# Optimization experiments

Hardware: AMD Instinct MI355X
Metric: run time of the kernel (lower is better)

Reference implementation:

```python
import jax, jax.numpy as jnp
import numpy as np

EPS = 1e-5

def layer_norm(x, w, b):
    mu = x.mean(-1, keepdims=True)
    var = x.var(-1, keepdims=True)
    return (x - mu) / jnp.sqrt(var + EPS) * w + b

def s5_forward(u, Lambda_re, Lambda_im, B_re, B_im, C_re, C_im, D, log_step):
    # u: [B, L, H]; diagonal S5 SSM with P complex states, ZOH discretization.
    Lam = (Lambda_re + 1j * Lambda_im).astype(jnp.complex64)          # [P]
    dt = jnp.exp(log_step).astype(jnp.complex64)                       # [P]
    Lam_bar = jnp.exp(Lam * dt)                                        # [P]
    Bc = (B_re + 1j * B_im).astype(jnp.complex64)                      # [P, H]
    B_bar = ((Lam_bar - 1.0) / Lam)[:, None] * Bc                      # [P, H]
    Bu = jnp.einsum('blh,ph->blp', u.astype(jnp.complex64), B_bar)     # [B, L, P]
    A = jnp.broadcast_to(Lam_bar, Bu.shape)                            # [B, L, P]

    def binop(e1, e2):
        a1, b1 = e1
        a2, b2 = e2
        return (a2 * a1, a2 * b1 + b2)

    _, xs = jax.lax.associative_scan(binop, (A, Bu), axis=1)           # [B, L, P]
    Cc = (C_re + 1j * C_im).astype(jnp.complex64)                      # [H, P]
    y = 2.0 * jnp.einsum('blp,hp->blh', xs, Cc).real + D * u           # [B, L, H]
    return y

def setup_inputs() -> dict:
    key = jax.random.key(0)
    ks = jax.random.split(key, 12)
    B, L, H, P = 4, 4096, 512, 512
    x = jax.random.normal(ks[0], (B, L, H), jnp.float32)
    # SSM params (HiPPO-like flavor: negative real part, spread imaginary part)
    Lambda_re = -(0.5 * jax.random.uniform(ks[1], (P,), jnp.float32) + 0.1)
    Lambda_im = jnp.pi * jnp.arange(P, dtype=jnp.float32)
    B_re = jax.random.normal(ks[2], (P, H), jnp.float32) / np.sqrt(2.0 * H)
    B_im = jax.random.normal(ks[3], (P, H), jnp.float32) / np.sqrt(2.0 * H)
    C_re = jax.random.normal(ks[4], (H, P), jnp.float32) / np.sqrt(P)
    C_im = jax.random.normal(ks[5], (H, P), jnp.float32) / np.sqrt(P)
    D = jax.random.normal(ks[6], (H,), jnp.float32)
    log_step = jax.random.uniform(ks[7], (P,), jnp.float32,
                                  minval=np.log(1e-3), maxval=np.log(1e-1))
    ln1_w = jnp.ones((H,), jnp.float32); ln1_b = jnp.zeros((H,), jnp.float32)
    ln2_w = jnp.ones((H,), jnp.float32); ln2_b = jnp.zeros((H,), jnp.float32)
    W_enc = jax.random.normal(ks[8], (2 * H, H), jnp.float32) / np.sqrt(H)
    W_dec = jax.random.normal(ks[9], (H, H), jnp.float32) / np.sqrt(H)
    return {"x": x, "ln1_w": ln1_w, "ln1_b": ln1_b,
            "Lambda_re": Lambda_re, "Lambda_im": Lambda_im,
            "B_re": B_re, "B_im": B_im, "C_re": C_re, "C_im": C_im,
            "D": D, "log_step": log_step,
            "ln2_w": ln2_w, "ln2_b": ln2_b, "W_enc": W_enc, "W_dec": W_dec}

def reference(x, ln1_w, ln1_b, Lambda_re, Lambda_im, B_re, B_im, C_re, C_im,
              D, log_step, ln2_w, ln2_b, W_enc, W_dec):
    fx = layer_norm(x, ln1_w, ln1_b)
    res = fx
    u = s5_forward(fx, Lambda_re, Lambda_im, B_re, B_im, C_re, C_im, D, log_step)
    h = jax.nn.gelu(u, approximate=False) + res  # eval mode: dropout = identity
    fx2 = layer_norm(h, ln2_w, ln2_b)
    e = fx2 @ W_enc.T                              # [B, L, 2H]
    a, g = jnp.split(e, 2, axis=-1)
    ff = a * jax.nn.gelu(g, approximate=False)     # GEGLU
    out = ff @ W_dec.T + fx2
    return out
```

## Files before the change

### kernel.cpp

```cpp
#include <hip/hip_runtime.h>
#include <math.h>

#define Bz 4
#define Lz 4096
#define Hz 512
#define Pz 512
#define Nz (Bz*Lz)
#define CL 32
#define NC (Lz/CL)
#define CS (Bz*NC*Pz)
#define EPSf 1e-5f

typedef unsigned short u16;
typedef unsigned int   u32;
typedef __attribute__((ext_vector_type(8))) short bf16x8;
typedef __attribute__((ext_vector_type(8))) short short8v;
typedef __attribute__((ext_vector_type(4))) float f32x4;

__device__ __forceinline__ float gelu_exact(float x){
    return 0.5f * x * (1.0f + erff(x * 0.70710678118654752f));
}
__device__ __forceinline__ u16 f2b(float f){
    union { float f; u32 u; } v; v.f = f;
    u32 u = v.u;
    u32 r = (u + 0x7FFFu + ((u >> 16) & 1u)) >> 16;
    return (u16)r;
}
__device__ __forceinline__ float b2f(u16 h){
    union { u32 u; float f; } v; v.u = ((u32)h) << 16; return v.f;
}

__device__ __forceinline__ void gload_lds16(const u16* g, u16* l){
    __builtin_amdgcn_global_load_lds(
        (const __attribute__((address_space(1))) void*)g,
        (__attribute__((address_space(3))) void*)l, 16, 0, 0);
}

__device__ __forceinline__ void load8(const float* p, float* v){
    f32x4 a = *(const f32x4*)p, c = *(const f32x4*)(p+4);
    #pragma unroll
    for (int j=0;j<4;++j){ v[j]=a[j]; v[4+j]=c[j]; }
}
__device__ __forceinline__ void load8(const u16* p, float* v){
    short8v s = *(const short8v*)p;
    #pragma unroll
    for (int j=0;j<8;++j) v[j] = b2f((u16)s[j]);
}

__global__ void setup_kernel(const float* __restrict__ Lre, const float* __restrict__ Lim,
                             const float* __restrict__ log_step,
                             float* __restrict__ prm){
    int p = blockIdx.x*blockDim.x + threadIdx.x;
    if (p >= Pz) return;
    float lr = Lre[p], li = Lim[p];
    float dt = expf(log_step[p]);
    float ar = lr*dt, ai = li*dt;
    float e = expf(ar);
    float Abr = e*cosf(ai), Abi = e*sinf(ai);
    prm[p]        = Abr;
    prm[Pz + p]   = Abi;
    float nr = Abr - 1.0f, ni = Abi;
    float d2 = lr*lr + li*li;
    prm[2*Pz + p] = (nr*lr + ni*li)/d2;
    prm[3*Pz + p] = (ni*lr - nr*li)/d2;
    float arC = ar*(float)CL, aiC = ai*(float)CL;
    float eC = expf(arC);
    prm[4*Pz + p] = eC*cosf(aiC);
    prm[5*Pz + p] = eC*sinf(aiC);
}

__global__ __launch_bounds__(256) void cvt_all(const float* __restrict__ B_re,
                                               const float* __restrict__ B_im,
                                               const float* __restrict__ C_re,
                                               const float* __restrict__ C_im,
                                               const float* __restrict__ W_enc,
                                               const float* __restrict__ W_dec,
                                               u16* __restrict__ Bcat,
                                               u16* __restrict__ Ccat,
                                               u16* __restrict__ Wenc,
                                               u16* __restrict__ Wdec){
    const int Q = 512*512;
    int i = blockIdx.x*256 + threadIdx.x;
    if (i < Q){ int p=i>>9, h=i&511; Bcat[(size_t)(2*p)*512 + h]   = f2b(B_re[i]); return; }
    i -= Q;
    if (i < Q){ int p=i>>9, h=i&511; Bcat[(size_t)(2*p+1)*512 + h] = f2b(B_im[i]); return; }
    i -= Q;
    if (i < Q){
        int h = i >> 9, p = i & 511;
        Ccat[(size_t)h*1024 + 2*p]     = f2b(C_re[i]);
        Ccat[(size_t)h*1024 + 2*p + 1] = f2b(-C_im[i]);
        return;
    }
    i -= Q;
    if (i < 2*Q){ Wenc[i] = f2b(W_enc[i]); return; }
    i -= 2*Q;
    Wdec[i] = f2b(W_dec[i]);
}

template<typename T>
__global__ __launch_bounds__(256) void ln_kernel(const T* __restrict__ in,
                                                 const float* __restrict__ w,
                                                 const float* __restrict__ b,
                                                 u16* __restrict__ ob){
    int row = blockIdx.x*4 + (threadIdx.x >> 6);
    int l = threadIdx.x & 63;
    float v[8];
    load8(in + (size_t)row*Hz + l*8, v);
    float s = 0.f, q = 0.f;
    #pragma unroll
    for (int j=0;j<8;++j){ s += v[j]; q += v[j]*v[j]; }
    #pragma unroll
    for (int o=32;o;o>>=1){ s += __shfl_xor(s,o); q += __shfl_xor(q,o); }
    float mu = s * (1.0f/512.0f);
    float rs = rsqrtf(q * (1.0f/512.0f) - mu*mu + EPSf);
    short8v o8;
    #pragma unroll
    for (int j=0;j<8;++j){
        int m = l*8 + j;
        o8[j] = (short)f2b((v[j]-mu)*rs*w[m] + b[m]);
    }
    *(short8v*)&ob[(size_t)row*Hz + l*8] = o8;
}

#define EY    1
#define ERES  2
#define EGLU  3
#define ESCAN 4

#define ATW (256*64)
#define BTW (128*64)
#define TBW (ATW+BTW)

__device__ __forceinline__ void stageA256v(const u16* __restrict__ src, int ld,
                                           int row0, int kt, u16* lds){
    int lane = threadIdx.x & 63, w = threadIdx.x >> 6;
    #pragma unroll
    for (int q=0;q<4;++q){
        int c = w + q*8;
        int r = c*8 + (lane >> 3);
        int colE = 8*((lane & 7) ^ ((lane >> 3) & 7));
        gload_lds16(src + (size_t)(row0 + r)*ld + kt + colE, lds + c*512);
    }
}
__device__ __forceinline__ void stageB128v(const u16* __restrict__ src, int ld,
                                           int row0, int kt, u16* lds){
    int lane = threadIdx.x & 63, w = threadIdx.x >> 6;
    #pragma unroll
    for (int q=0;q<2;++q){
        int c = w + q*8;
        int r = c*8 + (lane >> 3);
        int colE = 8*((lane & 7) ^ ((lane >> 3) & 7));
        gload_lds16(src + (size_t)(row0 + r)*ld + kt + colE, lds + c*512);
    }
}
__device__ __forceinline__ void stageBglu(const u16* __restrict__ Wenc, int fb,
                                          int kt, u16* lds){
    int lane = threadIdx.x & 63, w = threadIdx.x >> 6;
    #pragma unroll
    for (int q=0;q<2;++q){
        int c = w + q*8;
        int v = c*8 + (lane >> 3);
        int vf = v >> 4, r = v & 15;
        int grow = ((vf & 1) ? 512 : 0) + fb + (vf >> 1)*16 + r;
        int colE = 8*((lane & 7) ^ ((lane >> 3) & 7));
        gload_lds16(Wenc + (size_t)grow*512 + kt + colE, lds + c*512);
    }
}

template<int K, int EPI>
__global__ __launch_bounds__(512)
void gemmv(const u16* __restrict__ A, const u16* __restrict__ Bw, int M,
           u16* __restrict__ outB,
           const u16* __restrict__ fxB,
           const float* __restrict__ Dv,
           const u16* __restrict__ resB,
           float* __restrict__ outF,
           const float* __restrict__ prm,
           float* __restrict__ ERe,
           float* __restrict__ EIm)
{
    constexpr int NT = K/64;
    __shared__ u16 LDS[3*TBW];

    int nx = gridDim.x, ny = gridDim.y;
    int nwg = nx*ny;
    int lid = blockIdx.x + blockIdx.y*nx;
    int cpx = nwg >> 3;
    int gdx = (lid & 7)*cpx + (lid >> 3);
    int n0 = (gdx / ny) * 256;
    int mb = gdx % ny;
    int m0 = mb * 128;
    int fb = mb * 64;

    int l = threadIdx.x & 63;
    int w = threadIdx.x >> 6;
    int wm = w >> 1, wn = w & 1;
    int rb = wm*64, cb = wn*64;
    int lrow  = l & 15;
    int lcol0 = ((l >> 4)*8) ^ ((l & 7) << 3);
    int lcol1 = lcol0 ^ 32;

    f32x4 acc[4][4];
    #pragma unroll
    for (int i=0;i<4;++i)
        #pragma unroll
        for (int j=0;j<4;++j) acc[i][j] = (f32x4)(0.f);

    stageA256v(A, K, n0, 0, &LDS[0]);
    if (EPI==EGLU) stageBglu(Bw, fb, 0, &LDS[ATW]); else stageB128v(Bw, K, m0, 0, &LDS[ATW]);
    stageA256v(A, K, n0, 64, &LDS[TBW]);
    if (EPI==EGLU) stageBglu(Bw, fb, 64, &LDS[TBW+ATW]); else stageB128v(Bw, K, m0, 64, &LDS[TBW+ATW]);

    for (int T=0; T<NT; ++T){
        if (T == NT-1){ asm volatile("s_waitcnt vmcnt(0)" ::: "memory"); }
        else          { asm volatile("s_waitcnt vmcnt(6)" ::: "memory"); }
        __builtin_amdgcn_s_barrier();
        if (T+2 < NT){
            u16* buf = &LDS[((T+2)%3)*TBW];
            int ktn = (T+2)*64;
            stageA256v(A, K, n0, ktn, buf);
            if (EPI==EGLU) stageBglu(Bw, fb, ktn, buf+ATW); else stageB128v(Bw, K, m0, ktn, buf+ATW);
        }
        const u16* Ab = &LDS[(T%3)*TBW];
        const u16* Bb = Ab + ATW;
        bf16x8 a0[4], a1[4], b0[4], b1[4];
        #pragma unroll
        for (int f=0; f<4; ++f){
            a0[f] = *(const bf16x8*)&Ab[(rb + f*16 + lrow)*64 + lcol0];
            a1[f] = *(const bf16x8*)&Ab[(rb + f*16 + lrow)*64 + lcol1];
        }
        #pragma unroll
        for (int g=0; g<4; ++g){
            b0[g] = *(const bf16x8*)&Bb[(cb + g*16 + lrow)*64 + lcol0];
            b1[g] = *(const bf16x8*)&Bb[(cb + g*16 + lrow)*64 + lcol1];
        }
        __builtin_amdgcn_s_setprio(1);
        #pragma unroll
        for (int f=0; f<4; ++f)
            #pragma unroll
            for (int g=0; g<4; ++g){
                acc[f][g] = __builtin_amdgcn_mfma_f32_16x16x32_bf16(a0[f], b0[g], acc[f][g], 0,0,0);
                acc[f][g] = __builtin_amdgcn_mfma_f32_16x16x32_bf16(a1[f], b1[g], acc[f][g], 0,0,0);
            }
        __builtin_amdgcn_s_setprio(0);
    }

    int er = (l >> 4) * 4;
    int ec = l & 15;

    if (EPI == ESCAN){
        u16* gt = (u16*)LDS;
        __syncthreads();
        #pragma unroll
        for (int fm=0; fm<4; ++fm)
            #pragma unroll
            for (int g=0; g<4; ++g)
                #pragma unroll
                for (int q=0; q<4; ++q){
                    int rr = rb + fm*16 + er + q;
                    int cc = cb + g*16 + ec;
                    u16 hv = f2b(acc[fm][g][q]);
                    outB[(size_t)(n0 + rr)*M + (m0 + cc)] = hv;
                    gt[rr*128 + cc] = hv;
                }
        __syncthreads();
        int tid = threadIdx.x;
        int p = tid & 63, h = tid >> 6;
        int P = (m0 >> 1) + p;
        int b = n0 >> 12;
        int c = ((n0 & 4095) >> 5) + h;
        float Ar = prm[P], Ai = prm[Pz+P];
        float fre = prm[2*Pz+P], fim = prm[3*Pz+P];
        float xr = 0.f, xi = 0.f;
        int base = h*32*128 + 2*p;
        #pragma unroll 8
        for (int r = 0; r < 32; ++r){
            u32 v = *(const u32*)&gt[base + r*128];
            float gr = b2f((u16)(v & 0xffff));
            float gi = b2f((u16)(v >> 16));
            float br = fre*gr - fim*gi;
            float bi = fre*gi + fim*gr;
            float nr2 = Ar*xr - Ai*xi + br;
            float ni2 = Ar*xi + Ai*xr + bi;
            xr = nr2; xi = ni2;
        }
        size_t ci = ((size_t)(b*NC + c))*Pz + P;
        ERe[ci] = xr; EIm[ci] = xi;
    } else if (EPI == EGLU){
        #pragma unroll
        for (int fm=0; fm<4; ++fm)
            #pragma unroll
            for (int pr=0; pr<2; ++pr)
                #pragma unroll
                for (int q=0; q<4; ++q){
                    int n = n0 + rb + fm*16 + er + q;
                    int col = fb + (wn*2 + pr)*16 + ec;
                    float ffv = acc[fm][2*pr][q] * gelu_exact(acc[fm][2*pr+1][q]);
                    outB[(size_t)n*Hz + col] = f2b(ffv);
                }
    } else {
        #pragma unroll
        for (int fm=0; fm<4; ++fm)
            #pragma unroll
            for (int g=0; g<4; ++g)
                #pragma unroll
                for (int q=0; q<4; ++q){
                    int n = n0 + rb + fm*16 + er + q;
                    int m = m0 + cb + g*16 + ec;
                    float v = acc[fm][g][q];
                    if (EPI == EY){
                        size_t idx = (size_t)n*Hz + m;
                        float fxv = b2f(fxB[idx]);
                        float y = 2.0f*v + Dv[m]*fxv;
                        outB[idx] = f2b(gelu_exact(y) + fxv);
                    } else {
                        size_t idx = (size_t)n*Hz + m;
                        outF[idx] = v + b2f(resB[idx]);
                    }
                }
    }
}

__global__ __launch_bounds__(256) void scan_combine(const float* __restrict__ ERe,
                                                    const float* __restrict__ EIm,
                                                    const float* __restrict__ prm,
                                                    float* __restrict__ SinRe,
                                                    float* __restrict__ SinIm){
    int gt = blockIdx.x*256 + threadIdx.x;
    int b = gt / Pz, p = gt % Pz;
    float Ar = prm[4*Pz+p], Ai = prm[5*Pz+p];
    float Sr = 0.f, Si = 0.f;
    for (int c = 0; c < NC; ++c) {
        size_t idx = ((size_t)(b*NC + c))*Pz + p;
        SinRe[idx] = Sr; SinIm[idx] = Si;
        float er = ERe[idx], ei = EIm[idx];
        float nr = Ar*Sr - Ai*Si + er;
        float ni = Ar*Si + Ai*Sr + ei;
        Sr = nr; Si = ni;
    }
}

__global__ __launch_bounds__(64) void scan_phase2(u16* __restrict__ g,
                                                  const float* __restrict__ prm,
                                                  const float* __restrict__ SinRe,
                                                  const float* __restrict__ SinIm){
    int t = blockIdx.x;
    int ph = t & 1; t >>= 1;
    int c  = t % NC;
    int b  = t / NC;
    int p0 = ph*256 + threadIdx.x*4;
    int cbi = 2*p0;
    size_t base = ((size_t)(b*Lz + c*CL))*1024;
    size_t ci = ((size_t)(b*NC + c))*Pz + p0;
    float Ar[4], Ai[4], fr[4], fi[4], xr[4], xi[4];
    f32x4 sr4 = *(const f32x4*)&SinRe[ci];
    f32x4 si4 = *(const f32x4*)&SinIm[ci];
    #pragma unroll
    for (int j=0;j<4;++j){
        Ar[j]=prm[p0+j]; Ai[j]=prm[Pz+p0+j];
        fr[j]=prm[2*Pz+p0+j]; fi[j]=prm[3*Pz+p0+j];
        xr[j]=sr4[j]; xi[j]=si4[j];
    }
    for (int ll=0; ll<CL; ++ll){
        short8v v8 = *(const short8v*)&g[base + cbi];
        short8v o8;
        #pragma unroll
        for (int j=0;j<4;++j){
            float gr = b2f((u16)v8[2*j]), gi = b2f((u16)v8[2*j+1]);
            float br = fr[j]*gr - fi[j]*gi;
            float bi = fr[j]*gi + fi[j]*gr;
            float nr = Ar[j]*xr[j] - Ai[j]*xi[j] + br;
            float ni = Ar[j]*xi[j] + Ai[j]*xr[j] + bi;
            xr[j]=nr; xi[j]=ni;
            o8[2*j]   = (short)f2b(nr);
            o8[2*j+1] = (short)f2b(ni);
        }
        *(short8v*)&g[base + cbi] = o8;
        base += 1024;
    }
}

extern "C" void kernel_launch(void* const* d_in, const int* in_sizes, int n_in,
                              void* d_out, int out_size, void* d_ws, size_t ws_size,
                              hipStream_t stream) {
    const float* x        = (const float*)d_in[0];
    const float* ln1_w    = (const float*)d_in[1];
    const float* ln1_b    = (const float*)d_in[2];
    const float* Lre      = (const float*)d_in[3];
    const float* Lim      = (const float*)d_in[4];
    const float* B_re     = (const float*)d_in[5];
    const float* B_im     = (const float*)d_in[6];
    const float* C_re     = (const float*)d_in[7];
    const float* C_im     = (const float*)d_in[8];
    const float* Dv       = (const float*)d_in[9];
    const float* log_step = (const float*)d_in[10];
    const float* ln2_w    = (const float*)d_in[11];
    const float* ln2_b    = (const float*)d_in[12];
    const float* W_enc    = (const float*)d_in[13];
    const float* W_dec    = (const float*)d_in[14];
    float* out = (float*)d_out;

    const size_t NH = (size_t)Nz*Hz;
    char* W = (char*)d_ws;
    u16*   fxb  = (u16*)  (W);
    u16*   g    = (u16*)  (W + NH*2);
    u16*   hb   = (u16*)  (W + NH*6);
    u16*   fx2b = (u16*)  (W + NH*8);
    float* ERe  = (float*)(W + NH*10);
    float* EIm  = ERe + CS;
    float* SinRe= EIm + CS;
    float* SinIm= SinRe + CS;
    float* prm  = SinIm + CS;
    u16*   Bcat = (u16*)(prm + 6*Pz);
    u16*   Ccat = Bcat + 1024*512;
    u16*   Wenc = Ccat + 512*1024;
    u16*   Wdec = Wenc + 1024*512;

    setup_kernel<<<dim3(2), dim3(256), 0, stream>>>(Lre, Lim, log_step, prm);

    cvt_all<<<dim3(6*1024), dim3(256), 0, stream>>>(B_re, B_im, C_re, C_im, W_enc, W_dec,
                                                    Bcat, Ccat, Wenc, Wdec);

    ln_kernel<float><<<dim3(Nz/4), dim3(256), 0, stream>>>(x, ln1_w, ln1_b, fxb);

    gemmv<512,ESCAN><<<dim3(Nz/256, 1024/128), dim3(512), 0, stream>>>(
        fxb, Bcat, 1024, g, nullptr, nullptr, nullptr, nullptr, prm, ERe, EIm);

    scan_combine<<<dim3((Bz*Pz)/256), dim3(256), 0, stream>>>(ERe, EIm, prm, SinRe, SinIm);
    scan_phase2<<<dim3(Bz*NC*2), dim3(64), 0, stream>>>(g, prm, SinRe, SinIm);

    gemmv<1024,EY><<<dim3(Nz/256, 512/128), dim3(512), 0, stream>>>(
        g, Ccat, 512, hb, fxb, Dv, nullptr, nullptr, nullptr, nullptr, nullptr);

    ln_kernel<u16><<<dim3(Nz/4), dim3(256), 0, stream>>>(hb, ln2_w, ln2_b, fx2b);

    gemmv<512,EGLU><<<dim3(Nz/256, 1024/128), dim3(512), 0, stream>>>(
        fx2b, Wenc, 1024, fxb, nullptr, nullptr, nullptr, nullptr, nullptr, nullptr, nullptr);

    gemmv<512,ERES><<<dim3(Nz/256, 512/128), dim3(512), 0, stream>>>(
        fxb, Wdec, 512, nullptr, nullptr, nullptr, fx2b, out, nullptr, nullptr, nullptr);
}
```

Before: 169.2 us.

## Process two row tiles per GEGLU GEMM block, merge setup into conversion kernel

The GEGLU encoder GEMM now has each workgroup handle two consecutive 256-row tiles. The K loop runs across both tiles in one pipelined stream, and the first tile's GEGLU epilogue is written mid-loop before the accumulators are reset. This halves the grid and is meant to amortize pipeline fill and drain and the prologue cost, but the epilogue now stalls inside the pipeline. The setup kernel is folded into cvt_all as extra blocks to save a launch, and scan_combine uses 64-thread blocks to spread its 2048 serial threads over more CUs.

```diff
diff --git a/kernel.cpp b/kernel.cpp
--- a/kernel.cpp
+++ b/kernel.cpp
@@ -47,40 +47,43 @@
     for (int j=0;j<8;++j) v[j] = b2f((u16)s[j]);
 }
 
-__global__ void setup_kernel(const float* __restrict__ Lre, const float* __restrict__ Lim,
-                             const float* __restrict__ log_step,
-                             float* __restrict__ prm){
-    int p = blockIdx.x*blockDim.x + threadIdx.x;
-    if (p >= Pz) return;
-    float lr = Lre[p], li = Lim[p];
-    float dt = expf(log_step[p]);
-    float ar = lr*dt, ai = li*dt;
-    float e = expf(ar);
-    float Abr = e*cosf(ai), Abi = e*sinf(ai);
-    prm[p]        = Abr;
-    prm[Pz + p]   = Abi;
-    float nr = Abr - 1.0f, ni = Abi;
-    float d2 = lr*lr + li*li;
-    prm[2*Pz + p] = (nr*lr + ni*li)/d2;
-    prm[3*Pz + p] = (ni*lr - nr*li)/d2;
-    float arC = ar*(float)CL, aiC = ai*(float)CL;
-    float eC = expf(arC);
-    prm[4*Pz + p] = eC*cosf(aiC);
-    prm[5*Pz + p] = eC*sinf(aiC);
-}
-
 __global__ __launch_bounds__(256) void cvt_all(const float* __restrict__ B_re,
                                                const float* __restrict__ B_im,
                                                const float* __restrict__ C_re,
                                                const float* __restrict__ C_im,
                                                const float* __restrict__ W_enc,
                                                const float* __restrict__ W_dec,
+                                               const float* __restrict__ Lre,
+                                               const float* __restrict__ Lim,
+                                               const float* __restrict__ log_step,
                                                u16* __restrict__ Bcat,
                                                u16* __restrict__ Ccat,
                                                u16* __restrict__ Wenc,
-                                               u16* __restrict__ Wdec){
+                                               u16* __restrict__ Wdec,
+                                               float* __restrict__ prm){
     const int Q = 512*512;
-    int i = blockIdx.x*256 + threadIdx.x;
+    int blk = blockIdx.x;
+    if (blk >= 6*1024){
+        int p = (blk - 6*1024)*256 + threadIdx.x;
+        if (p >= Pz) return;
+        float lr = Lre[p], li = Lim[p];
+        float dt = expf(log_step[p]);
+        float ar = lr*dt, ai = li*dt;
+        float e = expf(ar);
+        float Abr = e*cosf(ai), Abi = e*sinf(ai);
+        prm[p]        = Abr;
+        prm[Pz + p]   = Abi;
+        float nr = Abr - 1.0f, ni = Abi;
+        float d2 = lr*lr + li*li;
+        prm[2*Pz + p] = (nr*lr + ni*li)/d2;
+        prm[3*Pz + p] = (ni*lr - nr*li)/d2;
+        float arC = ar*(float)CL, aiC = ai*(float)CL;
+        float eC = expf(arC);
+        prm[4*Pz + p] = eC*cosf(aiC);
+        prm[5*Pz + p] = eC*sinf(aiC);
+        return;
+    }
+    int i = blk*256 + threadIdx.x;
     if (i < Q){ int p=i>>9, h=i&511; Bcat[(size_t)(2*p)*512 + h]   = f2b(B_re[i]); return; }
     i -= Q;
     if (i < Q){ int p=i>>9, h=i&511; Bcat[(size_t)(2*p+1)*512 + h] = f2b(B_im[i]); return; }
@@ -180,6 +183,8 @@
            float* __restrict__ EIm)
 {
     constexpr int NT = K/64;
+    constexpr int NP = (EPI==EGLU) ? 2 : 1;
+    constexpr int TT = NT*NP;
     __shared__ u16 LDS[3*TBW];
 
     int nx = gridDim.x, ny = gridDim.y;
@@ -187,7 +192,7 @@
     int lid = blockIdx.x + blockIdx.y*nx;
     int cpx = nwg >> 3;
     int gdx = (lid & 7)*cpx + (lid >> 3);
-    int n0 = (gdx / ny) * 256;
+    int n0 = (gdx / ny) * 256 * NP;
     int mb = gdx % ny;
     int m0 = mb * 128;
     int fb = mb * 64;
@@ -199,6 +204,8 @@
     int lrow  = l & 15;
     int lcol0 = ((l >> 4)*8) ^ ((l & 7) << 3);
     int lcol1 = lcol0 ^ 32;
+    int er = (l >> 4) * 4;
+    int ec = l & 15;
 
     f32x4 acc[4][4];
     #pragma unroll
@@ -211,14 +218,16 @@
     stageA256v(A, K, n0, 64, &LDS[TBW]);
     if (EPI==EGLU) stageBglu(Bw, fb, 64, &LDS[TBW+ATW]); else stageB128v(Bw, K, m0, 64, &LDS[TBW+ATW]);
 
-    for (int T=0; T<NT; ++T){
-        if (T == NT-1){ asm volatile("s_waitcnt vmcnt(0)" ::: "memory"); }
+    for (int T=0; T<TT; ++T){
+        if (T == TT-1){ asm volatile("s_waitcnt vmcnt(0)" ::: "memory"); }
         else          { asm volatile("s_waitcnt vmcnt(6)" ::: "memory"); }
         __builtin_amdgcn_s_barrier();
-        if (T+2 < NT){
+        if (T+2 < TT){
             u16* buf = &LDS[((T+2)%3)*TBW];
-            int ktn = (T+2)*64;
-            stageA256v(A, K, n0, ktn, buf);
+            int t2 = T+2;
+            int ktn = (t2 % NT)*64;
+            int rowA = n0 + (t2/NT)*256;
+            stageA256v(A, K, rowA, ktn, buf);
             if (EPI==EGLU) stageBglu(Bw, fb, ktn, buf+ATW); else stageB128v(Bw, K, m0, ktn, buf+ATW);
         }
         const u16* Ab = &LDS[(T%3)*TBW];
@@ -243,10 +252,24 @@
                 acc[f][g] = __builtin_amdgcn_mfma_f32_16x16x32_bf16(a1[f], b1[g], acc[f][g], 0,0,0);
             }
         __builtin_amdgcn_s_setprio(0);
-    }
-
-    int er = (l >> 4) * 4;
-    int ec = l & 15;
+        if (EPI==EGLU && NP==2 && T == NT-1){
+            #pragma unroll
+            for (int fm=0; fm<4; ++fm)
+                #pragma unroll
+                for (int pr=0; pr<2; ++pr)
+                    #pragma unroll
+                    for (int q=0; q<4; ++q){
+                        int n = n0 + rb + fm*16 + er + q;
+                        int col = fb + (wn*2 + pr)*16 + ec;
+                        float ffv = acc[fm][2*pr][q] * gelu_exact(acc[fm][2*pr+1][q]);
+                        outB[(size_t)n*Hz + col] = f2b(ffv);
+                    }
+            #pragma unroll
+            for (int i=0;i<4;++i)
+                #pragma unroll
+                for (int j=0;j<4;++j) acc[i][j] = (f32x4)(0.f);
+        }
+    }
 
     if (EPI == ESCAN){
         u16* gt = (u16*)LDS;
@@ -287,13 +310,14 @@
         size_t ci = ((size_t)(b*NC + c))*Pz + P;
         ERe[ci] = xr; EIm[ci] = xi;
     } else if (EPI == EGLU){
+        int nb = n0 + (NP-1)*256;
         #pragma unroll
         for (int fm=0; fm<4; ++fm)
             #pragma unroll
             for (int pr=0; pr<2; ++pr)
                 #pragma unroll
                 for (int q=0; q<4; ++q){
-                    int n = n0 + rb + fm*16 + er + q;
+                    int n = nb + rb + fm*16 + er + q;
                     int col = fb + (wn*2 + pr)*16 + ec;
                     float ffv = acc[fm][2*pr][q] * gelu_exact(acc[fm][2*pr+1][q]);
                     outB[(size_t)n*Hz + col] = f2b(ffv);
@@ -321,12 +345,12 @@
     }
 }
 
-__global__ __launch_bounds__(256) void scan_combine(const float* __restrict__ ERe,
-                                                    const float* __restrict__ EIm,
-                                                    const float* __restrict__ prm,
-                                                    float* __restrict__ SinRe,
-                                                    float* __restrict__ SinIm){
-    int gt = blockIdx.x*256 + threadIdx.x;
+__global__ __launch_bounds__(64) void scan_combine(const float* __restrict__ ERe,
+                                                   const float* __restrict__ EIm,
+                                                   const float* __restrict__ prm,
+                                                   float* __restrict__ SinRe,
+                                                   float* __restrict__ SinIm){
+    int gt = blockIdx.x*64 + threadIdx.x;
     int b = gt / Pz, p = gt % Pz;
     float Ar = prm[4*Pz+p], Ai = prm[5*Pz+p];
     float Sr = 0.f, Si = 0.f;
@@ -416,17 +440,16 @@
     u16*   Wenc = Ccat + 512*1024;
     u16*   Wdec = Wenc + 1024*512;
 
-    setup_kernel<<<dim3(2), dim3(256), 0, stream>>>(Lre, Lim, log_step, prm);
-
-    cvt_all<<<dim3(6*1024), dim3(256), 0, stream>>>(B_re, B_im, C_re, C_im, W_enc, W_dec,
-                                                    Bcat, Ccat, Wenc, Wdec);
+    cvt_all<<<dim3(6*1024 + 2), dim3(256), 0, stream>>>(
+        B_re, B_im, C_re, C_im, W_enc, W_dec, Lre, Lim, log_step,
+        Bcat, Ccat, Wenc, Wdec, prm);
 
     ln_kernel<float><<<dim3(Nz/4), dim3(256), 0, stream>>>(x, ln1_w, ln1_b, fxb);
 
     gemmv<512,ESCAN><<<dim3(Nz/256, 1024/128), dim3(512), 0, stream>>>(
         fxb, Bcat, 1024, g, nullptr, nullptr, nullptr, nullptr, prm, ERe, EIm);
 
-    scan_combine<<<dim3((Bz*Pz)/256), dim3(256), 0, stream>>>(ERe, EIm, prm, SinRe, SinIm);
+    scan_combine<<<dim3((Bz*Pz)/64), dim3(64), 0, stream>>>(ERe, EIm, prm, SinRe, SinIm);
     scan_phase2<<<dim3(Bz*NC*2), dim3(64), 0, stream>>>(g, prm, SinRe, SinIm);
 
     gemmv<1024,EY><<<dim3(Nz/256, 512/128), dim3(512), 0, stream>>>(
@@ -434,7 +457,7 @@
 
     ln_kernel<u16><<<dim3(Nz/4), dim3(256), 0, stream>>>(hb, ln2_w, ln2_b, fx2b);
 
-    gemmv<512,EGLU><<<dim3(Nz/256, 1024/128), dim3(512), 0, stream>>>(
+    gemmv<512,EGLU><<<dim3(Nz/512, 1024/128), dim3(512), 0, stream>>>(
         fx2b, Wenc, 1024, fxb, nullptr, nullptr, nullptr, nullptr, nullptr, nullptr, nullptr);
 
     gemmv<512,ERES><<<dim3(Nz/256, 512/128), dim3(512), 0, stream>>>(
```

Result: no change. 166.7 us (-1.5%).
